# Performance work log

Hardware: AMD Instinct MI355X
Metric: run time of the kernel (lower is better)

## Reference

```python
import jax, jax.numpy as jnp
import numpy as np

LR = 0.1          # learning_rate
THRESHOLD = 0.1   # surprise_threshold (fixed; adaptive_threshold=False / eval path)
TEMP = 0.1        # temperature
EPS = 1e-6

B, S, DK, DV = 64, 1024, 128, 128


def setup_inputs() -> dict:
    key = jax.random.key(0)
    k1, k2 = jax.random.split(key)
    return {
        "memory": jnp.zeros((B, DV, DK), dtype=jnp.float32),
        "key": jax.random.normal(k1, (B, S, DK), dtype=jnp.float32),
        "value": jax.random.normal(k2, (B, S, DV), dtype=jnp.float32),
    }


def reference(memory, key, value):
    # memory: (B, DV, DK); key: (B, S, DK); value: (B, S, DV)
    # Sequential delta-rule fast-weight update with surprise gating.
    def step(mem, kv):
        k_t, v_t = kv                                  # (B, DK), (B, DV)
        k_n = k_t / (jnp.linalg.norm(k_t, axis=-1, keepdims=True) + EPS)
        predicted = jnp.einsum('bvk,bk->bv', mem, k_n)  # (B, DV)
        surprise = predicted - v_t                      # (B, DV)
        s_norm = jnp.linalg.norm(surprise, axis=-1, keepdims=True)  # (B, 1)
        gate = jax.nn.sigmoid((s_norm - THRESHOLD) / TEMP)          # (B, 1)
        # forget_term + lr*learn_term = (predicted + lr*surprise) outer k_n
        update = (predicted + LR * surprise)[:, :, None] * k_n[:, None, :]
        mem = mem - gate[:, :, None] * update
        return mem, gate

    # scan over the sequence axis
    kv_seq = (jnp.swapaxes(key, 0, 1), jnp.swapaxes(value, 0, 1))  # (S, B, *)
    mem_final, gates = jax.lax.scan(step, memory, kv_seq)
    gate_values = jnp.swapaxes(gates, 0, 1)  # (B, S, 1)
    return mem_final, gate_values
```

## Files before the change

### kernel.cpp

```cpp
#include <hip/hip_runtime.h>
#include <math.h>

#define B_    64
#define S_    1024
#define DK_   128
#define DV_   128
#define T_    16
#define NC_   (S_ / T_)
#define LR_   0.1f
#define LRP1_ 1.1f
#define THR_  0.1f
#define ITEMP_ 10.0f
#define EPS_  1e-6f

template<int CTRL>
__device__ __forceinline__ float dpp_add(float x) {
  int t = __builtin_amdgcn_update_dpp(0, __float_as_int(x), CTRL, 0xf, 0xf, true);
  return x + __int_as_float(t);
}
__device__ __forceinline__ float wave_sum64(float x) {
  x = dpp_add<0x111>(x); x = dpp_add<0x112>(x); x = dpp_add<0x114>(x);
  x = dpp_add<0x118>(x); x = dpp_add<0x142>(x); x = dpp_add<0x143>(x);
  return __int_as_float(__builtin_amdgcn_readlane(__float_as_int(x), 63));
}
__device__ __forceinline__ float row16_sum(float x) {
  x = dpp_add<0x111>(x); x = dpp_add<0x112>(x);
  x = dpp_add<0x114>(x); x = dpp_add<0x118>(x);
  return x;
}
__device__ __forceinline__ float quad_sum4(float x) {
  x = dpp_add<0xB1>(x); x = dpp_add<0x4E>(x); return x;
}
__device__ __forceinline__ float rdlane(float v, int l) {
  return __int_as_float(__builtin_amdgcn_readlane(__float_as_int(v), l));
}
__device__ __forceinline__ float dot4(float4 a, float4 b) {
  return fmaf(a.x, b.x, fmaf(a.y, b.y, fmaf(a.z, b.z, a.w * b.w)));
}
__device__ __forceinline__ void gll16(const float* g, float* l) {
  __builtin_amdgcn_global_load_lds(
      (const __attribute__((address_space(1))) unsigned int*)g,
      (__attribute__((address_space(3))) unsigned int*)l, 16, 0, 0);
}

__global__ __launch_bounds__(512, 2)
void sgm_kernel(const float* __restrict__ mem_in,
                const float* __restrict__ key,
                const float* __restrict__ value,
                float* __restrict__ out) {
  const int b    = blockIdx.x;
  const int tid  = threadIdx.x;
  const int g    = tid >> 4;
  const int h    = tid & 15;
  const int lane = tid & 63;
  const int wv   = tid >> 6;

  __shared__ __align__(16) float kS[2][T_][DK_];
  __shared__ __align__(16) float vS[2][T_][DV_];
  __shared__ __align__(16) float rawL[T_][DK_];
  __shared__ __align__(16) float cuL[T_][DK_];
  __shared__ __align__(16) float GT[T_][T_];
  __shared__ __align__(16) float gateL[S_];

  float4 mA[4], mB[4];
  {
    const float4* Mp = reinterpret_cast<const float4*>(mem_in + (size_t)b * DV_ * DK_);
    #pragma unroll
    for (int rr = 0; rr < 4; ++rr) {
      mA[rr] = Mp[(4*g + rr) * 32 + h];
      mB[rr] = Mp[(4*g + rr) * 32 + 16 + h];
    }
  }

  const float* kb = key   + (size_t)b * S_ * DK_;
  const float* vb = value + (size_t)b * S_ * DV_;

  auto stage = [&](int cc) {
    if (wv == 0 && lane < 32) {
      #pragma unroll
      for (int t = 0; t < T_; ++t)
        gll16(kb + (size_t)(cc * T_ + t) * DK_ + lane * 4, &kS[cc & 1][t][0]);
    }
    if (wv == 1 && lane < 32) {
      #pragma unroll
      for (int t = 0; t < T_; ++t)
        gll16(vb + (size_t)(cc * T_ + t) * DV_ + lane * 4, &vS[cc & 1][t][0]);
    }
  };

  auto applyUpdate = [&](int pb) {
    #pragma unroll
    for (int j = 0; j < T_; ++j) {
      const float4* kj = reinterpret_cast<const float4*>(&kS[pb][j][0]);
      const float4 kx = kj[h], ky = kj[16 + h];
      const float4 cu = *reinterpret_cast<const float4*>(&cuL[j][4 * g]);
      const float c[4] = {cu.x, cu.y, cu.z, cu.w};
      #pragma unroll
      for (int rr = 0; rr < 4; ++rr) {
        mA[rr].x = fmaf(-c[rr], kx.x, mA[rr].x); mA[rr].y = fmaf(-c[rr], kx.y, mA[rr].y);
        mA[rr].z = fmaf(-c[rr], kx.z, mA[rr].z); mA[rr].w = fmaf(-c[rr], kx.w, mA[rr].w);
        mB[rr].x = fmaf(-c[rr], ky.x, mB[rr].x); mB[rr].y = fmaf(-c[rr], ky.y, mB[rr].y);
        mB[rr].z = fmaf(-c[rr], ky.z, mB[rr].z); mB[rr].w = fmaf(-c[rr], ky.w, mB[rr].w);
      }
    }
  };

  stage(0);
  if (wv < 2) asm volatile("s_waitcnt vmcnt(0)" ::: "memory");
  __syncthreads();

  for (int c = 0; c < NC_; ++c) {
    const int cb = c & 1;

    if (c > 0) applyUpdate((c - 1) & 1);
    asm volatile("s_waitcnt lgkmcnt(0)" ::: "memory");
    __builtin_amdgcn_s_barrier();
    asm volatile("" ::: "memory");
    if (c + 1 < NC_) stage(c + 1);

    #pragma unroll
    for (int t = 0; t < T_; ++t) {
      const float4* kt = reinterpret_cast<const float4*>(&kS[cb][t][0]);
      const float4 kx = kt[h], ky = kt[16 + h];
      float a0 = dot4(mA[0], kx) + dot4(mB[0], ky);
      float a1 = dot4(mA[1], kx) + dot4(mB[1], ky);
      float a2 = dot4(mA[2], kx) + dot4(mB[2], ky);
      float a3 = dot4(mA[3], kx) + dot4(mB[3], ky);
      a0 = row16_sum(a0); a1 = row16_sum(a1);
      a2 = row16_sum(a2); a3 = row16_sum(a3);
      if (h == 15)
        *reinterpret_cast<float4*>(&rawL[t][4 * g]) = make_float4(a0, a1, a2, a3);
    }

    if (g < T_) {
      const float4* kt = reinterpret_cast<const float4*>(&kS[cb][g][0]);
      const float4 kx = kt[h], ky = kt[16 + h];
      float a = dot4(kx, kx) + dot4(ky, ky);
      a = row16_sum(a);
      if (h == 15) GT[g][g] = a;
    }

    {
      const int p = tid >> 2, c4 = tid & 3;
      if (p < 120) {
        int t = 1, pp = p;
        while (pp >= t) { pp -= t; ++t; }
        const int j = pp;
        const float4* kj4 = reinterpret_cast<const float4*>(&kS[cb][j][0]);
        const float4* kt4 = reinterpret_cast<const float4*>(&kS[cb][t][0]);
        float acc = 0.f;
        #pragma unroll
        for (int w = 0; w < 8; ++w)
          acc += dot4(kj4[c4 + 4 * w], kt4[c4 + 4 * w]);
        const float tot = quad_sum4(acc);
        if (c4 == 0) GT[t][j] = tot;
      }
    }

    asm volatile("s_waitcnt lgkmcnt(0)" ::: "memory");
    __builtin_amdgcn_s_barrier();
    asm volatile("" ::: "memory");

    {
      const int sj = lane & 15;
      float Gr[T_];
      float2 rv[T_], vv[T_];
      #pragma unroll
      for (int t = 0; t < T_; ++t) {
        Gr[t] = GT[t][sj];
        rv[t] = *reinterpret_cast<const float2*>(&rawL[t][2 * lane]);
        vv[t] = *reinterpret_cast<const float2*>(&vS[cb][t][2 * lane]);
      }
      const float rinv = 1.0f / (sqrtf(GT[sj][sj]) + EPS_);
      float cu0[T_], cu1[T_];
      #pragma unroll
      for (int t = 0; t < T_; ++t) {
        const float rin_t = rdlane(rinv, t);
        float y0 = 0.f, y1 = 0.f;
        #pragma unroll
        for (int j = 0; j < T_; ++j) {
          if (j < t) {
            const float gjt = rdlane(Gr[t], j);
            y0 = fmaf(gjt, cu0[j], y0);
            y1 = fmaf(gjt, cu1[j], y1);
          }
        }
        const float pred0 = rin_t * (rv[t].x - y0);
        const float pred1 = rin_t * (rv[t].y - y1);
        const float s0 = pred0 - vv[t].x, s1 = pred1 - vv[t].y;
        const float s2 = wave_sum64(fmaf(s0, s0, s1 * s1));
        const float gg = 1.0f / (1.0f + __expf((THR_ - sqrtf(s2)) * ITEMP_));
        if (tid == 0) gateL[c * T_ + t] = gg;
        const float ct = gg * rin_t;
        const float u0 = fmaf(LRP1_, pred0, -(LR_ * vv[t].x));
        const float u1 = fmaf(LRP1_, pred1, -(LR_ * vv[t].y));
        cu0[t] = ct * u0; cu1[t] = ct * u1;
        if (wv == 0)
          *reinterpret_cast<float2*>(&cuL[t][2 * lane]) = make_float2(cu0[t], cu1[t]);
      }
    }

    asm volatile("s_waitcnt lgkmcnt(0)" ::: "memory");
    if (wv < 2) asm volatile("s_waitcnt vmcnt(0)" ::: "memory");
    __builtin_amdgcn_s_barrier();
    asm volatile("" ::: "memory");
  }

  applyUpdate((NC_ - 1) & 1);

  {
    float4* Op = reinterpret_cast<float4*>(out + (size_t)b * DV_ * DK_);
    #pragma unroll
    for (int rr = 0; rr < 4; ++rr) {
      Op[(4*g + rr) * 32 + h] = mA[rr];
      Op[(4*g + rr) * 32 + 16 + h] = mB[rr];
    }
    float2* Gp = reinterpret_cast<float2*>(out + (size_t)B_ * DV_ * DK_ + (size_t)b * S_);
    Gp[tid] = reinterpret_cast<const float2*>(gateL)[tid];
  }
}

extern "C" void kernel_launch(void* const* d_in, const int* in_sizes, int n_in,
                              void* d_out, int out_size, void* d_ws, size_t ws_size,
                              hipStream_t stream) {
  const float* mem = (const float*)d_in[0];
  const float* key = (const float*)d_in[1];
  const float* val = (const float*)d_in[2];
  float* out = (float*)d_out;
  sgm_kernel<<<B_, 512, 0, stream>>>(mem, key, val, out);
}
```

Before: 663.3 us.

## Cache key half-rows in registers, pad LDS rows, run gate solve on one wave

Each thread now preloads its first-half key float4 for all 16 timesteps of a chunk into registers and reuses it for both the prediction dot products and the next chunk's rank-1 memory update, so that half of the key data is read from LDS once per chunk instead of twice. The key and value LDS tiles get padded rows, meant to reduce bank conflicts. The serial per-timestep gate/triangular solve is restricted to wave 0, which stops seven waves from doing the same work redundantly. The 64 extra registers per thread may pressure occupancy under launch_bounds(512,2) and could cause spills. The wave-0 path also reads rawL and vS per step rather than prefetching them.

```diff
diff --git a/kernel.cpp b/kernel.cpp
--- a/kernel.cpp
+++ b/kernel.cpp
@@ -7,6 +7,7 @@
 #define DV_   128
 #define T_    16
 #define NC_   (S_ / T_)
+#define KP_   (DK_ + 4)
 #define LR_   0.1f
 #define LRP1_ 1.1f
 #define THR_  0.1f
@@ -55,8 +56,8 @@
   const int lane = tid & 63;
   const int wv   = tid >> 6;
 
-  __shared__ __align__(16) float kS[2][T_][DK_];
-  __shared__ __align__(16) float vS[2][T_][DV_];
+  __shared__ __align__(16) float kS[2][T_][KP_];
+  __shared__ __align__(16) float vS[2][T_][KP_];
   __shared__ __align__(16) float rawL[T_][DK_];
   __shared__ __align__(16) float cuL[T_][DK_];
   __shared__ __align__(16) float GT[T_][T_];
@@ -88,19 +89,25 @@
     }
   };
 
+  float4 kxR[16];
+
   auto applyUpdate = [&](int pb) {
     #pragma unroll
     for (int j = 0; j < T_; ++j) {
       const float4* kj = reinterpret_cast<const float4*>(&kS[pb][j][0]);
-      const float4 kx = kj[h], ky = kj[16 + h];
+      const float4 ky = kj[16 + h];
       const float4 cu = *reinterpret_cast<const float4*>(&cuL[j][4 * g]);
-      const float c[4] = {cu.x, cu.y, cu.z, cu.w};
+      const float cc[4] = {cu.x, cu.y, cu.z, cu.w};
       #pragma unroll
       for (int rr = 0; rr < 4; ++rr) {
-        mA[rr].x = fmaf(-c[rr], kx.x, mA[rr].x); mA[rr].y = fmaf(-c[rr], kx.y, mA[rr].y);
-        mA[rr].z = fmaf(-c[rr], kx.z, mA[rr].z); mA[rr].w = fmaf(-c[rr], kx.w, mA[rr].w);
-        mB[rr].x = fmaf(-c[rr], ky.x, mB[rr].x); mB[rr].y = fmaf(-c[rr], ky.y, mB[rr].y);
-        mB[rr].z = fmaf(-c[rr], ky.z, mB[rr].z); mB[rr].w = fmaf(-c[rr], ky.w, mB[rr].w);
+        mA[rr].x = fmaf(-cc[rr], kxR[j].x, mA[rr].x);
+        mA[rr].y = fmaf(-cc[rr], kxR[j].y, mA[rr].y);
+        mA[rr].z = fmaf(-cc[rr], kxR[j].z, mA[rr].z);
+        mA[rr].w = fmaf(-cc[rr], kxR[j].w, mA[rr].w);
+        mB[rr].x = fmaf(-cc[rr], ky.x, mB[rr].x);
+        mB[rr].y = fmaf(-cc[rr], ky.y, mB[rr].y);
+        mB[rr].z = fmaf(-cc[rr], ky.z, mB[rr].z);
+        mB[rr].w = fmaf(-cc[rr], ky.w, mB[rr].w);
       }
     }
   };
@@ -113,6 +120,11 @@
     const int cb = c & 1;
 
     if (c > 0) applyUpdate((c - 1) & 1);
+
+    #pragma unroll
+    for (int t = 0; t < T_; ++t)
+      kxR[t] = reinterpret_cast<const float4*>(&kS[cb][t][0])[h];
+
     asm volatile("s_waitcnt lgkmcnt(0)" ::: "memory");
     __builtin_amdgcn_s_barrier();
     asm volatile("" ::: "memory");
@@ -120,12 +132,11 @@
 
     #pragma unroll
     for (int t = 0; t < T_; ++t) {
-      const float4* kt = reinterpret_cast<const float4*>(&kS[cb][t][0]);
-      const float4 kx = kt[h], ky = kt[16 + h];
-      float a0 = dot4(mA[0], kx) + dot4(mB[0], ky);
-      float a1 = dot4(mA[1], kx) + dot4(mB[1], ky);
-      float a2 = dot4(mA[2], kx) + dot4(mB[2], ky);
-      float a3 = dot4(mA[3], kx) + dot4(mB[3], ky);
+      const float4 ky = reinterpret_cast<const float4*>(&kS[cb][t][0])[16 + h];
+      float a0 = dot4(mA[0], kxR[t]) + dot4(mB[0], ky);
+      float a1 = dot4(mA[1], kxR[t]) + dot4(mB[1], ky);
+      float a2 = dot4(mA[2], kxR[t]) + dot4(mB[2], ky);
+      float a3 = dot4(mA[3], kxR[t]) + dot4(mB[3], ky);
       a0 = row16_sum(a0); a1 = row16_sum(a1);
       a2 = row16_sum(a2); a3 = row16_sum(a3);
       if (h == 15)
@@ -161,16 +172,11 @@
     __builtin_amdgcn_s_barrier();
     asm volatile("" ::: "memory");
 
-    {
+    if (wv == 0) {
       const int sj = lane & 15;
       float Gr[T_];
-      float2 rv[T_], vv[T_];
-      #pragma unroll
-      for (int t = 0; t < T_; ++t) {
-        Gr[t] = GT[t][sj];
-        rv[t] = *reinterpret_cast<const float2*>(&rawL[t][2 * lane]);
-        vv[t] = *reinterpret_cast<const float2*>(&vS[cb][t][2 * lane]);
-      }
+      #pragma unroll
+      for (int t = 0; t < T_; ++t) Gr[t] = GT[t][sj];
       const float rinv = 1.0f / (sqrtf(GT[sj][sj]) + EPS_);
       float cu0[T_], cu1[T_];
       #pragma unroll
@@ -185,18 +191,19 @@
             y1 = fmaf(gjt, cu1[j], y1);
           }
         }
-        const float pred0 = rin_t * (rv[t].x - y0);
-        const float pred1 = rin_t * (rv[t].y - y1);
-        const float s0 = pred0 - vv[t].x, s1 = pred1 - vv[t].y;
+        const float2 rv = *reinterpret_cast<const float2*>(&rawL[t][2 * lane]);
+        const float2 vv = *reinterpret_cast<const float2*>(&vS[cb][t][2 * lane]);
+        const float pred0 = rin_t * (rv.x - y0);
+        const float pred1 = rin_t * (rv.y - y1);
+        const float s0 = pred0 - vv.x, s1 = pred1 - vv.y;
         const float s2 = wave_sum64(fmaf(s0, s0, s1 * s1));
         const float gg = 1.0f / (1.0f + __expf((THR_ - sqrtf(s2)) * ITEMP_));
-        if (tid == 0) gateL[c * T_ + t] = gg;
+        if (lane == 0) gateL[c * T_ + t] = gg;
         const float ct = gg * rin_t;
-        const float u0 = fmaf(LRP1_, pred0, -(LR_ * vv[t].x));
-        const float u1 = fmaf(LRP1_, pred1, -(LR_ * vv[t].y));
+        const float u0 = fmaf(LRP1_, pred0, -(LR_ * vv.x));
+        const float u1 = fmaf(LRP1_, pred1, -(LR_ * vv.y));
         cu0[t] = ct * u0; cu1[t] = ct * u1;
-        if (wv == 0)
-          *reinterpret_cast<float2*>(&cuL[t][2 * lane]) = make_float2(cu0[t], cu1[t]);
+        *reinterpret_cast<float2*>(&cuL[t][2 * lane]) = make_float2(cu0[t], cu1[t]);
       }
     }
 
```

After: 589.2 us. 11.2% less time.
